# Optimization experiments

Hardware: AMD Instinct MI355X
Metric: run time of the kernel (lower is better)

Reference implementation:

```python
import jax, jax.numpy as jnp
import numpy as np

B, T = 64, 256
E = 300          # embedding_size
H = 512          # hidden_num
L = 9            # label_size
V = 30000        # vocab_size
S = 30000        # sentence_size


def setup_inputs() -> dict:
    key = jax.random.key(0)
    ks = jax.random.split(key, 14)
    D = 2 * E
    inp = {
        "text": jax.random.randint(ks[0], (B, T), 0, V, dtype=jnp.int32),
        "sentence": jax.random.randint(ks[1], (B, T), 0, S, dtype=jnp.int32),
        "labels": jax.random.randint(ks[2], (B, T), 0, L, dtype=jnp.int32),
        "word_emb": jax.random.normal(ks[3], (V, E), jnp.float32) * 0.05,
        "sent_emb": jax.random.normal(ks[4], (S, E), jnp.float32) * 0.05,
        "Wk_f": jax.random.normal(ks[5], (D, 4 * H), jnp.float32) / np.sqrt(D).astype(np.float32),
        "Wr_f": jax.random.normal(ks[6], (H, 4 * H), jnp.float32) / np.sqrt(H).astype(np.float32),
        "b_f": jnp.zeros((4 * H,), jnp.float32),
        "Wk_b": jax.random.normal(ks[7], (D, 4 * H), jnp.float32) / np.sqrt(D).astype(np.float32),
        "Wr_b": jax.random.normal(ks[8], (H, 4 * H), jnp.float32) / np.sqrt(H).astype(np.float32),
        "b_b": jnp.zeros((4 * H,), jnp.float32),
        "Wd": jax.random.normal(ks[9], (2 * H, L), jnp.float32) / np.sqrt(2 * H).astype(np.float32),
        "bd": jnp.zeros((L,), jnp.float32),
        "trans": jax.random.uniform(ks[10], (L, L), jnp.float32),
    }
    return inp


def lstm(x, Wk, Wr, b):
    # x: [B,T,D]; Keras LSTM gate order i,f,g,o; sigmoid recurrent act, tanh act.
    xz = jnp.einsum('btd,dk->btk', x, Wk) + b  # one big GEMM for all timesteps
    h0 = jnp.zeros((x.shape[0], Wr.shape[0]), x.dtype)

    def step(carry, z_t):
        h, c = carry
        z = z_t + h @ Wr
        i, f, g, o = jnp.split(z, 4, axis=-1)
        c = jax.nn.sigmoid(f) * c + jax.nn.sigmoid(i) * jnp.tanh(g)
        h = jax.nn.sigmoid(o) * jnp.tanh(c)
        return (h, c), h

    _, hs = jax.lax.scan(step, (h0, h0), jnp.swapaxes(xz, 0, 1))
    return jnp.swapaxes(hs, 0, 1)  # [B,T,H]


def crf_log_likelihood(logits, labels, mask, trans):
    maskf = mask.astype(logits.dtype)
    # unary score of the gold path
    unary = jnp.take_along_axis(logits, labels[..., None], axis=-1)[..., 0]  # [B,T]
    unary = jnp.sum(unary * maskf, axis=-1)
    # binary (transition) score
    binary = trans[labels[:, :-1], labels[:, 1:]]  # [B,T-1]
    binary = jnp.sum(binary * maskf[:, 1:], axis=-1)
    # forward algorithm (log partition), masked steps carry alpha
    logits_tm = jnp.swapaxes(logits, 0, 1)  # [T,B,L]
    mask_tm = jnp.swapaxes(mask, 0, 1)

    def step(alpha, inputs):
        logit_t, m_t = inputs
        new = jax.nn.logsumexp(alpha[:, :, None] + trans[None], axis=1) + logit_t
        return jnp.where(m_t[:, None], new, alpha), None

    alpha, _ = jax.lax.scan(step, logits_tm[0], (logits_tm[1:], mask_tm[1:]))
    log_norm = jax.nn.logsumexp(alpha, axis=-1)
    return unary + binary - log_norm


def crf_decode(logits, trans, mask):
    b, t, l = logits.shape
    logits_tm = jnp.swapaxes(logits, 0, 1)
    mask_tm = jnp.swapaxes(mask, 0, 1)
    ident = jnp.broadcast_to(jnp.arange(l)[None], (b, l))

    def step(alpha, inputs):
        logit_t, m_t = inputs
        score = alpha[:, :, None] + trans[None]      # [B,L,L]
        bp = jnp.argmax(score, axis=1)               # [B,L]
        new = jnp.max(score, axis=1) + logit_t
        alpha = jnp.where(m_t[:, None], new, alpha)
        bp = jnp.where(m_t[:, None], bp, ident)      # identity through padding
        return alpha, bp

    alpha, bps = jax.lax.scan(step, logits_tm[0], (logits_tm[1:], mask_tm[1:]))
    last = jnp.argmax(alpha, axis=-1)  # [B]

    def back(tag, bp):
        prev = jnp.take_along_axis(bp, tag[:, None], axis=1)[:, 0]
        return prev, prev

    _, tags = jax.lax.scan(back, last, bps, reverse=True)  # [T-1,B], original time order
    tags = jnp.concatenate([tags, last[None]], axis=0)     # [T,B]
    return jnp.swapaxes(tags, 0, 1).astype(jnp.int32)


def reference(text, sentence, labels, word_emb, sent_emb, Wk_f, Wr_f, b_f,
              Wk_b, Wr_b, b_b, Wd, bd, trans):
    x = jnp.concatenate([word_emb[text], sent_emb[sentence]], axis=-1)  # [B,T,2E]
    hf = lstm(x, Wk_f, Wr_f, b_f)
    hb = lstm(x[:, ::-1], Wk_b, Wr_b, b_b)[:, ::-1]
    h = jnp.concatenate([hf, hb], axis=-1)  # [B,T,2H]
    logits = h @ Wd + bd                    # [B,T,L]
    text_lens = jnp.sum((text != 0).astype(jnp.int32), axis=-1)
    mask = jnp.arange(T)[None, :] < text_lens[:, None]
    log_likelihood = crf_log_likelihood(logits, labels, mask, trans)
    pred_tags = crf_decode(logits, trans, mask)
    return logits, text_lens, log_likelihood, pred_tags
```

## Files before the change

kernel.cpp:

```cpp
#include <hip/hip_runtime.h>
#include <hip/hip_bf16.h>
#include <math.h>

#define BB 64
#define TT 256
#define EE 300
#define DD 600
#define KP 608
#define HH 512
#define G4 2048
#define LL 9
#define NT (BB*TT)

typedef __attribute__((ext_vector_type(8))) short short8;
typedef __attribute__((ext_vector_type(4))) float floatx4;

#define XZF_OFF  ((size_t)0)
#define XZ_BYTES ((size_t)NT * G4 * 2)
#define XZB_OFF  (XZF_OFF + XZ_BYTES)
#define HSR_OFF  (XZB_OFF + XZ_BYTES)
#define HS_BYTES ((size_t)NT * HH * 2)
#define HSF_OFF  (HSR_OFF)
#define HSB_OFF  (HSR_OFF + HS_BYTES)
#define XG_OFF   (HSR_OFF)
#define WKT_OFF  (HSR_OFF + 19922944)
#define WRT_OFF  (HSR_OFF + (size_t)2 * HS_BYTES)
#define BK_OFF   (WRT_OFF + 4194304)
#define FAST_OFF (BK_OFF + 524288)
#define EX_BYTES ((size_t)2 * 2 * BB * HH * 4)
#define FLAGS_OFF (FAST_OFF + 524288)
#define WDT_OFF  XZF_OFF

#define OUT_LOGITS 0
#define OUT_LENS   (BB*TT*LL)
#define OUT_LL     (OUT_LENS + BB)
#define OUT_TAGS   (OUT_LL + BB)

__global__ __launch_bounds__(256) void prep_xg(
    const int* __restrict__ text, const int* __restrict__ sent,
    const float* __restrict__ wemb, const float* __restrict__ semb,
    __hip_bfloat16* __restrict__ xg)
{
    int n = blockIdx.x;
    int ti = text[n], si = sent[n];
    __hip_bfloat16* o = xg + (size_t)n * KP;
    for (int k = threadIdx.x; k < KP; k += 256) {
        float v = 0.f;
        if (k < EE)      v = wemb[(size_t)ti * EE + k];
        else if (k < DD) v = semb[(size_t)si * EE + (k - EE)];
        o[k] = __float2bfloat16(v);
    }
}

__global__ __launch_bounds__(256) void transpose_w(
    const float* __restrict__ Wf, const float* __restrict__ Wb,
    __hip_bfloat16* __restrict__ outT, int Din, int Dpad)
{
    int dir = blockIdx.z;
    const float* W = dir ? Wb : Wf;
    __hip_bfloat16* o = outT + (size_t)dir * G4 * Dpad;
    int n0 = blockIdx.x * 64, d0 = blockIdx.y * 64;
    __shared__ float tile[64][65];
    int c = threadIdx.x & 63, r4 = threadIdx.x >> 6;
    #pragma unroll
    for (int rr = 0; rr < 64; rr += 4) {
        int d = d0 + rr + r4;
        tile[rr + r4][c] = (d < Din) ? W[(size_t)d * G4 + n0 + c] : 0.f;
    }
    __syncthreads();
    #pragma unroll
    for (int rr = 0; rr < 64; rr += 4) {
        int n = n0 + rr + r4;
        int d = d0 + c;
        if (d < Dpad) o[(size_t)n * Dpad + d] = __float2bfloat16(tile[c][rr + r4]);
    }
}

__global__ __launch_bounds__(256) void prep_wdT(
    const float* __restrict__ Wd, __hip_bfloat16* __restrict__ WdT)
{
    for (int i = threadIdx.x + blockIdx.x * 256; i < 16 * 1024; i += gridDim.x * 256) {
        int nn = i >> 10, k = i & 1023;
        WdT[i] = __float2bfloat16(nn < LL ? Wd[(size_t)k * LL + nn] : 0.f);
    }
}

__global__ __launch_bounds__(256) void embed_gemm(
    const __hip_bfloat16* __restrict__ xg,
    const __hip_bfloat16* __restrict__ WkT,
    const float* __restrict__ b_f, const float* __restrict__ b_b,
    __hip_bfloat16* __restrict__ xz_f, __hip_bfloat16* __restrict__ xz_b)
{
    int dir = blockIdx.z;
    const __hip_bfloat16* wt = WkT + (size_t)dir * G4 * KP;
    const float* bias = dir ? b_b : b_f;
    __hip_bfloat16* xz = dir ? xz_b : xz_f;

    int n0 = blockIdx.x * 128;
    int c0 = blockIdx.y * 64;
    int wave = threadIdx.x >> 6, lane = threadIdx.x & 63;
    int m0 = (wave & 1) * 64;
    int nn0 = (wave >> 1) * 32;
    int lm = lane & 15, lk8 = (lane >> 4) * 8;

    const short8 *ap[4], *bp2[2];
    #pragma unroll
    for (int i = 0; i < 4; ++i)
        ap[i] = (const short8*)(xg + (size_t)(n0 + m0 + i*16 + lm) * KP + lk8);
    #pragma unroll
    for (int i = 0; i < 2; ++i)
        bp2[i] = (const short8*)(wt + (size_t)(c0 + nn0 + i*16 + lm) * KP + lk8);

    floatx4 acc[4][2] = {};
    for (int kc = 0; kc < KP/32; ++kc) {
        short8 a0 = ap[0][kc*4], a1 = ap[1][kc*4], a2 = ap[2][kc*4], a3 = ap[3][kc*4];
        short8 b0 = bp2[0][kc*4], b1 = bp2[1][kc*4];
        acc[0][0] = __builtin_amdgcn_mfma_f32_16x16x32_bf16(a0, b0, acc[0][0], 0,0,0);
        acc[0][1] = __builtin_amdgcn_mfma_f32_16x16x32_bf16(a0, b1, acc[0][1], 0,0,0);
        acc[1][0] = __builtin_amdgcn_mfma_f32_16x16x32_bf16(a1, b0, acc[1][0], 0,0,0);
        acc[1][1] = __builtin_amdgcn_mfma_f32_16x16x32_bf16(a1, b1, acc[1][1], 0,0,0);
        acc[2][0] = __builtin_amdgcn_mfma_f32_16x16x32_bf16(a2, b0, acc[2][0], 0,0,0);
        acc[2][1] = __builtin_amdgcn_mfma_f32_16x16x32_bf16(a2, b1, acc[2][1], 0,0,0);
        acc[3][0] = __builtin_amdgcn_mfma_f32_16x16x32_bf16(a3, b0, acc[3][0], 0,0,0);
        acc[3][1] = __builtin_amdgcn_mfma_f32_16x16x32_bf16(a3, b1, acc[3][1], 0,0,0);
    }

    int lr = (lane >> 4) * 4;
    #pragma unroll
    for (int ni = 0; ni < 2; ++ni) {
        int col = c0 + nn0 + ni*16 + lm;
        float bs = bias[col];
        #pragma unroll
        for (int mi = 0; mi < 4; ++mi) {
            #pragma unroll
            for (int r = 0; r < 4; ++r) {
                int row = n0 + m0 + mi*16 + lr + r;
                xz[(size_t)row * G4 + col] = __float2bfloat16(acc[mi][ni][r] + bs);
            }
        }
    }
}

__device__ __forceinline__ void load16_sc0(const unsigned long long* base,
                                           int tid, unsigned long long* v)
{
    #pragma unroll
    for (int q = 0; q < 16; ++q) {
        const unsigned long long* ap = base + tid + 256 * q;
        asm volatile("global_load_dwordx2 %0, %1, off sc0"
                     : "=v"(v[q]) : "v"(ap));
    }
    asm volatile("s_waitcnt vmcnt(0)" ::: "memory");
}

__device__ __forceinline__ void store_sc0(unsigned long long* p,
                                          unsigned long long val)
{
    asm volatile("global_store_dwordx2 %0, %1, off sc0"
                 :: "v"(p), "v"(val) : "memory");
}

__device__ __forceinline__ unsigned load_u32_sc0(const unsigned* p)
{
    unsigned r;
    asm volatile("global_load_dword %0, %1, off sc0\n\ts_waitcnt vmcnt(0)"
                 : "=v"(r) : "v"(p) : "memory");
    return r;
}

__device__ __forceinline__ void store_u32_sc0(unsigned* p, unsigned v)
{
    asm volatile("global_store_dword %0, %1, off sc0" :: "v"(p), "v"(v) : "memory");
}

__device__ __forceinline__ void block_barrier_raw()
{
    asm volatile("" ::: "memory");
    __builtin_amdgcn_sched_barrier(0);
    __builtin_amdgcn_s_barrier();
    __builtin_amdgcn_sched_barrier(0);
    asm volatile("" ::: "memory");
}

__global__ __launch_bounds__(256, 1) void lstm_coop(
    const __hip_bfloat16* __restrict__ xz_f, const __hip_bfloat16* __restrict__ xz_b,
    const __hip_bfloat16* __restrict__ WrT,
    unsigned* __restrict__ bk,
    unsigned* __restrict__ fast,
    unsigned* __restrict__ flags,
    __hip_bfloat16* __restrict__ hs_f, __hip_bfloat16* __restrict__ hs_b)
{
    int blk = blockIdx.x;
    int g = blk & 7;
    int member = blk >> 3;
    int dir = g >> 2;
    int r0 = (g & 3) * 16;
    int h0 = member * 16;
    int tid = threadIdx.x;
    int gate = tid >> 6, lane = tid & 63;
    int lm = lane & 15, lk8 = (lane >> 4) * 8;

    const __hip_bfloat16* xz = dir ? xz_b : xz_f;
    __hip_bfloat16* hs = dir ? hs_b : hs_f;
    const __hip_bfloat16* wrt = WrT + (size_t)dir * G4 * HH;
    unsigned* bkd = bk + (size_t)dir * 2 * BB * HH;
    unsigned* fsd = fast + (size_t)dir * 2 * BB * HH;
    const unsigned* gfl = flags + (g << 5);
    unsigned* myflag = flags + (g << 5) + member;

    short8 bfrag[16];
    {
        const short8* wp = (const short8*)(wrt + (size_t)(gate*HH + h0 + lm) * HH + lk8);
        #pragma unroll
        for (int kc = 0; kc < 16; ++kc) bfrag[kc] = wp[kc*4];
    }

    __shared__ unsigned short htile[16][520];
    __shared__ float zbuf[4][16][17];

    int er = tid >> 3, ec = (tid & 7) * 2;
    float c0st = 0.f, c1st = 0.f;
    int zr = (lane >> 4) * 4;

    unsigned short xz_cur[4], xz_nxt[4];
    {
        int tok0 = dir ? (TT - 1) : 0;
        #pragma unroll
        for (int r = 0; r < 4; ++r) {
            int n = (r0 + zr + r) * TT + tok0;
            xz_cur[r] = *(const unsigned short*)(xz + (size_t)n * G4 + gate*HH + h0 + lm);
        }
    }

    bool fastok = true;
    int fallcnt = 0;

    for (int t = 0; t < TT; ++t) {
        int tok = dir ? (TT - 1 - t) : t;
        size_t soff = (size_t)(t & 1) * BB * HH + (size_t)r0 * HH;
        const unsigned long long pat =
            ((unsigned long long)(unsigned)t << 48) |
            ((unsigned long long)(unsigned)t << 16);

        unsigned long long v[16];
        bool ok = false;
        if (fastok) {
            const unsigned long long* fsrc = (const unsigned long long*)(fsd + soff);
            load16_sc0(fsrc, tid, v);
            unsigned long long bad = 0;
            #pragma unroll
            for (int q = 0; q < 16; ++q)
                bad |= (v[q] ^ pat) & 0xFFFF0000FFFF0000ULL;
            if (__all(bad == 0)) {
                ok = true;
            } else {
                unsigned need = (unsigned)t;
                bool flagok = false;
                for (int spin = 0; spin < 96; ++spin) {
                    unsigned f = load_u32_sc0(gfl + (lane & 31));
                    if (__all(f >= need)) { flagok = true; break; }
                    __builtin_amdgcn_s_sleep(2);
                }
                if (flagok) {
                    load16_sc0(fsrc, tid, v);
                    bad = 0;
                    #pragma unroll
                    for (int q = 0; q < 16; ++q)
                        bad |= (v[q] ^ pat) & 0xFFFF0000FFFF0000ULL;
                    if (__all(bad == 0)) ok = true;
                }
                if (!ok) { if (++fallcnt >= 3) fastok = false; }
            }
        }
        if (!ok) {
            const unsigned long long* bsrc = (const unsigned long long*)(bkd + soff);
            for (;;) {
                #pragma unroll
                for (int q = 0; q < 16; ++q)
                    v[q] = __hip_atomic_load(bsrc + tid + 256*q,
                            __ATOMIC_RELAXED, __HIP_MEMORY_SCOPE_AGENT);
                unsigned long long bad = 0;
                #pragma unroll
                for (int q = 0; q < 16; ++q)
                    bad |= (v[q] ^ pat) & 0xFFFF0000FFFF0000ULL;
                if (bad == 0) break;
                __builtin_amdgcn_s_sleep(2);
            }
        }

        #pragma unroll
        for (int q = 0; q < 16; ++q) {
            unsigned lo = (unsigned)(v[q] & 0xffffu);
            unsigned hi = (unsigned)((v[q] >> 32) & 0xffffu);
            *(unsigned*)&htile[q][tid * 2] = lo | (hi << 16);
        }
        __syncthreads();

        if (t + 1 < TT) {
            int tokn = dir ? (TT - 2 - t) : (t + 1);
            #pragma unroll
            for (int r = 0; r < 4; ++r) {
                int n = (r0 + zr + r) * TT + tokn;
                xz_nxt[r] = *(const unsigned short*)(xz + (size_t)n * G4 + gate*HH + h0 + lm);
            }
        }

        floatx4 acc = {};
        #pragma unroll
        for (int kc = 0; kc < 16; ++kc) {
            short8 a = *(const short8*)&htile[lm][kc * 32 + lk8];
            acc = __builtin_amdgcn_mfma_f32_16x16x32_bf16(a, bfrag[kc], acc, 0,0,0);
        }

        #pragma unroll
        for (int r = 0; r < 4; ++r) {
            float xv = __bfloat162float(__builtin_bit_cast(__hip_bfloat16, xz_cur[r]));
            zbuf[gate][zr + r][lm] = acc[r] + xv;
        }

        asm volatile("s_waitcnt lgkmcnt(0)" ::: "memory");
        block_barrier_raw();

        if (tid < 128) {
            float zi0 = zbuf[0][er][ec],   zi1 = zbuf[0][er][ec+1];
            float zf0 = zbuf[1][er][ec],   zf1 = zbuf[1][er][ec+1];
            float zg0 = zbuf[2][er][ec],   zg1 = zbuf[2][er][ec+1];
            float zo0 = zbuf[3][er][ec],   zo1 = zbuf[3][er][ec+1];
            float si0 = 1.f/(1.f+__expf(-zi0)), si1 = 1.f/(1.f+__expf(-zi1));
            float sf0 = 1.f/(1.f+__expf(-zf0)), sf1 = 1.f/(1.f+__expf(-zf1));
            float so0 = 1.f/(1.f+__expf(-zo0)), so1 = 1.f/(1.f+__expf(-zo1));
            c0st = sf0 * c0st + si0 * tanhf(zg0);
            c1st = sf1 * c1st + si1 * tanhf(zg1);
            float h0v = so0 * tanhf(c0st);
            float h1v = so1 * tanhf(c1st);
            unsigned u0 = (unsigned)__builtin_bit_cast(unsigned short, __float2bfloat16(h0v));
            unsigned u1 = (unsigned)__builtin_bit_cast(unsigned short, __float2bfloat16(h1v));
            unsigned tg = (unsigned)(t + 1) << 16;
            unsigned long long pay =
                ((unsigned long long)(tg | u1) << 32) | (unsigned long long)(tg | u0);
            size_t eoff = (size_t)((t+1) & 1) * BB * HH + (size_t)(r0 + er) * HH + h0 + ec;
            store_sc0((unsigned long long*)(fsd + eoff), pay);
            asm volatile("s_waitcnt vmcnt(0)" ::: "memory");
            __hip_atomic_store((unsigned long long*)(bkd + eoff), pay,
                               __ATOMIC_RELAXED, __HIP_MEMORY_SCOPE_AGENT);
            *(unsigned*)(hs + ((size_t)(r0 + er) * TT + tok) * HH + h0 + ec) =
                u0 | (u1 << 16);
        }
        block_barrier_raw();
        if (tid == 0)
            store_u32_sc0(myflag, (unsigned)(t + 1));

        #pragma unroll
        for (int r = 0; r < 4; ++r) xz_cur[r] = xz_nxt[r];
    }
}

__global__ __launch_bounds__(256) void logits_kernel(
    const __hip_bfloat16* __restrict__ hs_f, const __hip_bfloat16* __restrict__ hs_b,
    const __hip_bfloat16* __restrict__ WdT, const float* __restrict__ bd,
    float* __restrict__ out)
{
    int n0 = blockIdx.x * 64;
    int wave = threadIdx.x >> 6, lane = threadIdx.x & 63;
    int lm = lane & 15, lk8 = (lane >> 4) * 8;
    int nw = n0 + wave * 16;
    const short8* af = (const short8*)(hs_f + (size_t)(nw + lm) * HH + lk8);
    const short8* ab = (const short8*)(hs_b + (size_t)(nw + lm) * HH + lk8);
    const short8* bw = (const short8*)(WdT + (size_t)lm * 1024 + lk8);
    floatx4 acc = {};
    #pragma unroll
    for (int kc = 0; kc < 16; ++kc) {
        acc = __builtin_amdgcn_mfma_f32_16x16x32_bf16(af[kc*4], bw[kc*4], acc, 0,0,0);
        acc = __builtin_amdgcn_mfma_f32_16x16x32_bf16(ab[kc*4], bw[(kc+16)*4], acc, 0,0,0);
    }
    if (lm < LL) {
        float bv = bd[lm];
        #pragma unroll
        for (int r = 0; r < 4; ++r) {
            int n = nw + (lane >> 4) * 4 + r;
            out[(size_t)n * LL + lm] = acc[r] + bv;
        }
    }
}

__global__ __launch_bounds__(256) void crf_kernel(
    const float* __restrict__ logits, const int* __restrict__ text,
    const int* __restrict__ labels, const float* __restrict__ trans,
    float* __restrict__ out_lens, float* __restrict__ out_ll,
    float* __restrict__ out_tags)
{
    int b = blockIdx.x, tid = threadIdx.x;
    const float* lg = logits + (size_t)b * TT * LL;
    const int* lab = labels + b * TT;

    __shared__ float lgs[TT * LL];
    __shared__ float trs[81];
    __shared__ unsigned char bps[255 * LL + 1];
    __shared__ float partial[256];
    __shared__ int ired[256];
    __shared__ float tagf[TT];

    for (int i = tid; i < TT * LL; i += 256) lgs[i] = lg[i];
    if (tid < 81) trs[tid] = trans[tid];
    ired[tid] = (text[b * TT + tid] != 0) ? 1 : 0;
    __syncthreads();
    for (int s = 128; s > 0; s >>= 1) {
        if (tid < s) ired[tid] += ired[tid + s];
        __syncthreads();
    }
    int len = ired[0];
    if (tid == 0) out_lens[b] = (float)len;

    float up = 0.f;
    for (int t = tid; t < TT; t += 256) {
        float m = (t < len) ? 1.f : 0.f;
        up += m * lgs[t * LL + lab[t]];
        if (t >= 1) up += m * trs[lab[t - 1] * LL + lab[t]];
    }
    partial[tid] = up;
    __syncthreads();
    for (int s = 128; s > 0; s >>= 1) {
        if (tid < s) partial[tid] += partial[tid + s];
        __syncthreads();
    }

    if (tid < 64) {
        int lane = tid;
        int j = (lane < LL) ? lane : 0;
        float trj[LL];
        #pragma unroll
        for (int i = 0; i < LL; ++i) trj[i] = trs[i * LL + j];
        float alpha = lgs[j];
        float vit = alpha;
        for (int t = 1; t < TT; ++t) {
            bool m = t < len;
            float lgv = lgs[t * LL + j];
            float ta[LL];
            float mx = -1e30f, bv = -1e30f; int bi = 0;
            #pragma unroll
            for (int i = 0; i < LL; ++i) {
                float av = __shfl(alpha, i);
                float vv = __shfl(vit, i);
                ta[i] = av + trj[i];
                mx = fmaxf(mx, ta[i]);
                float sv = vv + trj[i];
                if (sv > bv) { bv = sv; bi = i; }
            }
            float s = 0.f;
            #pragma unroll
            for (int i = 0; i < LL; ++i) s += __expf(ta[i] - mx);
            float newa = mx + __logf(s) + lgv;
            float newv = bv + lgv;
            if (m) { alpha = newa; vit = newv; }
            if (lane < LL) bps[(t - 1) * LL + lane] = (unsigned char)(m ? bi : lane);
        }
        float aX[LL], vX[LL];
        #pragma unroll
        for (int i = 0; i < LL; ++i) { aX[i] = __shfl(alpha, i); vX[i] = __shfl(vit, i); }
        if (lane == 0) {
            float mx = -1e30f;
            #pragma unroll
            for (int i = 0; i < LL; ++i) mx = fmaxf(mx, aX[i]);
            float s = 0.f;
            #pragma unroll
            for (int i = 0; i < LL; ++i) s += __expf(aX[i] - mx);
            out_ll[b] = partial[0] - (mx + __logf(s));

            float bvv = vX[0]; int last = 0;
            #pragma unroll
            for (int i = 1; i < LL; ++i) if (vX[i] > bvv) { bvv = vX[i]; last = i; }
            tagf[TT - 1] = (float)last;
            int tg = last;
            for (int s2 = TT - 2; s2 >= 0; --s2) {
                tg = bps[s2 * LL + tg];
                tagf[s2] = (float)tg;
            }
        }
    }
    __syncthreads();
    out_tags[b * TT + tid] = tagf[tid];
}

extern "C" void kernel_launch(void* const* d_in, const int* in_sizes, int n_in,
                              void* d_out, int out_size, void* d_ws, size_t ws_size,
                              hipStream_t stream)
{
    const int*   text  = (const int*)d_in[0];
    const int*   sent  = (const int*)d_in[1];
    const int*   labels= (const int*)d_in[2];
    const float* wemb  = (const float*)d_in[3];
    const float* semb  = (const float*)d_in[4];
    const float* Wk_f  = (const float*)d_in[5];
    const float* Wr_f  = (const float*)d_in[6];
    const float* b_f   = (const float*)d_in[7];
    const float* Wk_b  = (const float*)d_in[8];
    const float* Wr_b  = (const float*)d_in[9];
    const float* b_b   = (const float*)d_in[10];
    const float* Wd    = (const float*)d_in[11];
    const float* bd    = (const float*)d_in[12];
    const float* trans = (const float*)d_in[13];
    float* out = (float*)d_out;

    char* ws = (char*)d_ws;
    __hip_bfloat16* xz_f = (__hip_bfloat16*)(ws + XZF_OFF);
    __hip_bfloat16* xz_b = (__hip_bfloat16*)(ws + XZB_OFF);
    __hip_bfloat16* hs_f = (__hip_bfloat16*)(ws + HSF_OFF);
    __hip_bfloat16* hs_b = (__hip_bfloat16*)(ws + HSB_OFF);
    __hip_bfloat16* xg   = (__hip_bfloat16*)(ws + XG_OFF);
    __hip_bfloat16* WkT  = (__hip_bfloat16*)(ws + WKT_OFF);
    __hip_bfloat16* WrT  = (__hip_bfloat16*)(ws + WRT_OFF);
    unsigned*       bk   = (unsigned*)(ws + BK_OFF);
    unsigned*       fast = (unsigned*)(ws + FAST_OFF);
    unsigned*       flg  = (unsigned*)(ws + FLAGS_OFF);
    __hip_bfloat16* WdT  = (__hip_bfloat16*)(ws + WDT_OFF);

    prep_xg <<<NT,  256, 0, stream>>>(text, sent, wemb, semb, xg);
    transpose_w<<<dim3(G4/64, (KP+63)/64, 2), 256, 0, stream>>>(Wk_f, Wk_b, WkT, DD, KP);
    transpose_w<<<dim3(G4/64, HH/64, 2),      256, 0, stream>>>(Wr_f, Wr_b, WrT, HH, HH);
    hipMemsetAsync(ws + BK_OFF, 0, 2 * EX_BYTES + 1024, stream);

    embed_gemm<<<dim3(NT/128, G4/64, 2), 256, 0, stream>>>(
        xg, WkT, b_f, b_b, xz_f, xz_b);

    {
        void* args[] = { (void*)&xz_f, (void*)&xz_b, (void*)&WrT,
                         (void*)&bk, (void*)&fast, (void*)&flg,
                         (void*)&hs_f, (void*)&hs_b };
        hipLaunchCooperativeKernel((const void*)lstm_coop, dim3(256), dim3(256),
                                   args, 0, stream);
    }

    prep_wdT<<<16, 256, 0, stream>>>(Wd, WdT);
    logits_kernel<<<NT/64, 256, 0, stream>>>(hs_f, hs_b, WdT, bd, out + OUT_LOGITS);
    crf_kernel<<<BB, 256, 0, stream>>>(out + OUT_LOGITS, text, labels, trans,
                                       out + OUT_LENS, out + OUT_LL, out + OUT_TAGS);
}
```

Before: 1.533 ms.

## Repartition LSTM recurrence into fewer, wider blocks of 512 threads

The cooperative LSTM kernel moves from 256 blocks of 256 threads, each owning 16 hidden units, to 64 blocks of 512 threads, each owning 64 hidden units. Every wave now issues two MFMA chains over 32 hidden columns, and all threads take part in the gate nonlinearities. With 8 members per group instead of 32, fewer blocks have to publish and poll per timestep, which is meant to cut cross-block synchronisation latency. In exchange each block does more serial work per step and holds more registers for weights. The fast-path fallback counter also now resets after a successful step.

```diff
diff --git a/kernel.cpp b/kernel.cpp
--- a/kernel.cpp
+++ b/kernel.cpp
@@ -141,12 +141,12 @@
     }
 }
 
-__device__ __forceinline__ void load16_sc0(const unsigned long long* base,
-                                           int tid, unsigned long long* v)
-{
-    #pragma unroll
-    for (int q = 0; q < 16; ++q) {
-        const unsigned long long* ap = base + tid + 256 * q;
+__device__ __forceinline__ void load8_sc0(const unsigned long long* base,
+                                          int tid, unsigned long long* v)
+{
+    #pragma unroll
+    for (int q = 0; q < 8; ++q) {
+        const unsigned long long* ap = base + tid + 512 * q;
         asm volatile("global_load_dwordx2 %0, %1, off sc0"
                      : "=v"(v[q]) : "v"(ap));
     }
@@ -182,7 +182,7 @@
     asm volatile("" ::: "memory");
 }
 
-__global__ __launch_bounds__(256, 1) void lstm_coop(
+__global__ __launch_bounds__(512, 2) void lstm_coop(
     const __hip_bfloat16* __restrict__ xz_f, const __hip_bfloat16* __restrict__ xz_b,
     const __hip_bfloat16* __restrict__ WrT,
     unsigned* __restrict__ bk,
@@ -195,10 +195,13 @@
     int member = blk >> 3;
     int dir = g >> 2;
     int r0 = (g & 3) * 16;
-    int h0 = member * 16;
     int tid = threadIdx.x;
-    int gate = tid >> 6, lane = tid & 63;
+    int wave = tid >> 6, lane = tid & 63;
+    int gate = wave >> 1;
+    int chunk = wave & 1;
     int lm = lane & 15, lk8 = (lane >> 4) * 8;
+    int zr = (lane >> 4) * 4;
+    int hbase = member * 64 + chunk * 32;
 
     const __hip_bfloat16* xz = dir ? xz_b : xz_f;
     __hip_bfloat16* hs = dir ? hs_b : hs_f;
@@ -208,28 +211,34 @@
     const unsigned* gfl = flags + (g << 5);
     unsigned* myflag = flags + (g << 5) + member;
 
-    short8 bfrag[16];
+    short8 bfragA[16], bfragB[16];
     {
-        const short8* wp = (const short8*)(wrt + (size_t)(gate*HH + h0 + lm) * HH + lk8);
-        #pragma unroll
-        for (int kc = 0; kc < 16; ++kc) bfrag[kc] = wp[kc*4];
+        const short8* wpA = (const short8*)(wrt +
+            (size_t)(gate*HH + hbase + lm) * HH + lk8);
+        const short8* wpB = (const short8*)(wrt +
+            (size_t)(gate*HH + hbase + 16 + lm) * HH + lk8);
+        #pragma unroll
+        for (int kc = 0; kc < 16; ++kc) { bfragA[kc] = wpA[kc*4]; bfragB[kc] = wpB[kc*4]; }
     }
 
     __shared__ unsigned short htile[16][520];
-    __shared__ float zbuf[4][16][17];
-
-    int er = tid >> 3, ec = (tid & 7) * 2;
+    __shared__ float zbuf[4][16][66];
+
+    int er = tid >> 5;
+    int ec = (tid & 31) * 2;
     float c0st = 0.f, c1st = 0.f;
-    int zr = (lane >> 4) * 4;
-
-    unsigned short xz_cur[4], xz_nxt[4];
+
+    unsigned short xz_cur[8], xz_nxt[8];
     {
         int tok0 = dir ? (TT - 1) : 0;
         #pragma unroll
-        for (int r = 0; r < 4; ++r) {
-            int n = (r0 + zr + r) * TT + tok0;
-            xz_cur[r] = *(const unsigned short*)(xz + (size_t)n * G4 + gate*HH + h0 + lm);
-        }
+        for (int ni = 0; ni < 2; ++ni)
+            #pragma unroll
+            for (int r = 0; r < 4; ++r) {
+                int n = (r0 + zr + r) * TT + tok0;
+                xz_cur[ni*4 + r] = *(const unsigned short*)(
+                    xz + (size_t)n * G4 + gate*HH + hbase + ni*16 + lm);
+            }
     }
 
     bool fastok = true;
@@ -242,14 +251,14 @@
             ((unsigned long long)(unsigned)t << 48) |
             ((unsigned long long)(unsigned)t << 16);
 
-        unsigned long long v[16];
+        unsigned long long v[8];
         bool ok = false;
         if (fastok) {
             const unsigned long long* fsrc = (const unsigned long long*)(fsd + soff);
-            load16_sc0(fsrc, tid, v);
+            load8_sc0(fsrc, tid, v);
             unsigned long long bad = 0;
             #pragma unroll
-            for (int q = 0; q < 16; ++q)
+            for (int q = 0; q < 8; ++q)
                 bad |= (v[q] ^ pat) & 0xFFFF0000FFFF0000ULL;
             if (__all(bad == 0)) {
                 ok = true;
@@ -257,71 +266,81 @@
                 unsigned need = (unsigned)t;
                 bool flagok = false;
                 for (int spin = 0; spin < 96; ++spin) {
-                    unsigned f = load_u32_sc0(gfl + (lane & 31));
+                    unsigned f = load_u32_sc0(gfl + (lane & 7));
                     if (__all(f >= need)) { flagok = true; break; }
                     __builtin_amdgcn_s_sleep(2);
                 }
                 if (flagok) {
-                    load16_sc0(fsrc, tid, v);
+                    load8_sc0(fsrc, tid, v);
                     bad = 0;
                     #pragma unroll
-                    for (int q = 0; q < 16; ++q)
+                    for (int q = 0; q < 8; ++q)
                         bad |= (v[q] ^ pat) & 0xFFFF0000FFFF0000ULL;
                     if (__all(bad == 0)) ok = true;
                 }
-                if (!ok) { if (++fallcnt >= 3) fastok = false; }
-            }
+            }
+            if (ok) fallcnt = 0;
+            else if (++fallcnt >= 3) fastok = false;
         }
         if (!ok) {
             const unsigned long long* bsrc = (const unsigned long long*)(bkd + soff);
             for (;;) {
                 #pragma unroll
-                for (int q = 0; q < 16; ++q)
-                    v[q] = __hip_atomic_load(bsrc + tid + 256*q,
+                for (int q = 0; q < 8; ++q)
+                    v[q] = __hip_atomic_load(bsrc + tid + 512*q,
                             __ATOMIC_RELAXED, __HIP_MEMORY_SCOPE_AGENT);
                 unsigned long long bad = 0;
                 #pragma unroll
-                for (int q = 0; q < 16; ++q)
+                for (int q = 0; q < 8; ++q)
                     bad |= (v[q] ^ pat) & 0xFFFF0000FFFF0000ULL;
                 if (bad == 0) break;
                 __builtin_amdgcn_s_sleep(2);
             }
         }
 
-        #pragma unroll
-        for (int q = 0; q < 16; ++q) {
-            unsigned lo = (unsigned)(v[q] & 0xffffu);
-            unsigned hi = (unsigned)((v[q] >> 32) & 0xffffu);
-            *(unsigned*)&htile[q][tid * 2] = lo | (hi << 16);
+        {
+            int srow = tid >> 8, scol = (tid & 255) * 2;
+            #pragma unroll
+            for (int q = 0; q < 8; ++q) {
+                unsigned lo = (unsigned)(v[q] & 0xffffu);
+                unsigned hi = (unsigned)((v[q] >> 32) & 0xffffu);
+                *(unsigned*)&htile[2*q + srow][scol] = lo | (hi << 16);
+            }
         }
         __syncthreads();
 
         if (t + 1 < TT) {
             int tokn = dir ? (TT - 2 - t) : (t + 1);
             #pragma unroll
-            for (int r = 0; r < 4; ++r) {
-                int n = (r0 + zr + r) * TT + tokn;
-                xz_nxt[r] = *(const unsigned short*)(xz + (size_t)n * G4 + gate*HH + h0 + lm);
-            }
-        }
-
-        floatx4 acc = {};
+            for (int ni = 0; ni < 2; ++ni)
+                #pragma unroll
+                for (int r = 0; r < 4; ++r) {
+                    int n = (r0 + zr + r) * TT + tokn;
+                    xz_nxt[ni*4 + r] = *(const unsigned short*)(
+                        xz + (size_t)n * G4 + gate*HH + hbase + ni*16 + lm);
+                }
+        }
+
+        floatx4 accA = {}, accB = {};
         #pragma unroll
         for (int kc = 0; kc < 16; ++kc) {
             short8 a = *(const short8*)&htile[lm][kc * 32 + lk8];
-            acc = __builtin_amdgcn_mfma_f32_16x16x32_bf16(a, bfrag[kc], acc, 0,0,0);
+            accA = __builtin_amdgcn_mfma_f32_16x16x32_bf16(a, bfragA[kc], accA, 0,0,0);
+            accB = __builtin_amdgcn_mfma_f32_16x16x32_bf16(a, bfragB[kc], accB, 0,0,0);
         }
 
         #pragma unroll
         for (int r = 0; r < 4; ++r) {
-            float xv = __bfloat162float(__builtin_bit_cast(__hip_bfloat16, xz_cur[r]));
-            zbuf[gate][zr + r][lm] = acc[r] + xv;
+            float xvA = __bfloat162float(__builtin_bit_cast(__hip_bfloat16, xz_cur[r]));
+            float xvB = __bfloat162float(__builtin_bit_cast(__hip_bfloat16, xz_cur[4 + r]));
+            zbuf[gate][zr + r][chunk*32 + lm]      = accA[r] + xvA;
+            zbuf[gate][zr + r][chunk*32 + 16 + lm] = accB[r] + xvB;
         }
 
         asm volatile("s_waitcnt lgkmcnt(0)" ::: "memory");
         block_barrier_raw();
 
-        if (tid < 128) {
+        {
             float zi0 = zbuf[0][er][ec],   zi1 = zbuf[0][er][ec+1];
             float zf0 = zbuf[1][er][ec],   zf1 = zbuf[1][er][ec+1];
             float zg0 = zbuf[2][er][ec],   zg1 = zbuf[2][er][ec+1];
@@ -338,12 +357,13 @@
             unsigned tg = (unsigned)(t + 1) << 16;
             unsigned long long pay =
                 ((unsigned long long)(tg | u1) << 32) | (unsigned long long)(tg | u0);
-            size_t eoff = (size_t)((t+1) & 1) * BB * HH + (size_t)(r0 + er) * HH + h0 + ec;
+            size_t eoff = (size_t)((t+1) & 1) * BB * HH
+                        + (size_t)(r0 + er) * HH + member*64 + ec;
             store_sc0((unsigned long long*)(fsd + eoff), pay);
             asm volatile("s_waitcnt vmcnt(0)" ::: "memory");
             __hip_atomic_store((unsigned long long*)(bkd + eoff), pay,
                                __ATOMIC_RELAXED, __HIP_MEMORY_SCOPE_AGENT);
-            *(unsigned*)(hs + ((size_t)(r0 + er) * TT + tok) * HH + h0 + ec) =
+            *(unsigned*)(hs + ((size_t)(r0 + er) * TT + tok) * HH + member*64 + ec) =
                 u0 | (u1 << 16);
         }
         block_barrier_raw();
@@ -351,7 +371,7 @@
             store_u32_sc0(myflag, (unsigned)(t + 1));
 
         #pragma unroll
-        for (int r = 0; r < 4; ++r) xz_cur[r] = xz_nxt[r];
+        for (int i = 0; i < 8; ++i) xz_cur[i] = xz_nxt[i];
     }
 }
 
@@ -526,7 +546,7 @@
         void* args[] = { (void*)&xz_f, (void*)&xz_b, (void*)&WrT,
                          (void*)&bk, (void*)&fast, (void*)&flg,
                          (void*)&hs_f, (void*)&hs_b };
-        hipLaunchCooperativeKernel((const void*)lstm_coop, dim3(256), dim3(256),
+        hipLaunchCooperativeKernel((const void*)lstm_coop, dim3(64), dim3(512),
                                    args, 0, stream);
     }
 
```

Result: slower. 2.737 ms (+78.6%).

## Use flag-gated packed bf16 exchange with dwordx4 loads in LSTM recurrence

Applied to the files above, without the earlier changes.

The fast path of the persistent LSTM recurrence now waits on per-group step flags first, then reads a packed bf16 h buffer with no embedded step tags using four 16-byte loads per thread. The old path read sixteen 8-byte tagged words and validated them. The gate nonlinearity is also spread over all 256 threads, one column each, with lane shuffles to pair outputs, where before 128 threads handled two columns each. The aim is to halve exchange traffic and shorten the per-step critical path. Correctness now depends on flag ordering, since data stores must be visible before the flag store, and the polling is tighter.

```diff
diff --git a/kernel.cpp b/kernel.cpp
--- a/kernel.cpp
+++ b/kernel.cpp
@@ -14,6 +14,7 @@
 
 typedef __attribute__((ext_vector_type(8))) short short8;
 typedef __attribute__((ext_vector_type(4))) float floatx4;
+typedef __attribute__((ext_vector_type(4))) unsigned uintx4;
 
 #define XZF_OFF  ((size_t)0)
 #define XZ_BYTES ((size_t)NT * G4 * 2)
@@ -141,23 +142,15 @@
     }
 }
 
-__device__ __forceinline__ void load16_sc0(const unsigned long long* base,
-                                           int tid, unsigned long long* v)
-{
-    #pragma unroll
-    for (int q = 0; q < 16; ++q) {
-        const unsigned long long* ap = base + tid + 256 * q;
-        asm volatile("global_load_dwordx2 %0, %1, off sc0"
+__device__ __forceinline__ void load4x16_sc0(const char* base, int tid, uintx4* v)
+{
+    #pragma unroll
+    for (int q = 0; q < 4; ++q) {
+        const char* ap = base + (size_t)(tid + 256 * q) * 16;
+        asm volatile("global_load_dwordx4 %0, %1, off sc0"
                      : "=v"(v[q]) : "v"(ap));
     }
     asm volatile("s_waitcnt vmcnt(0)" ::: "memory");
-}
-
-__device__ __forceinline__ void store_sc0(unsigned long long* p,
-                                          unsigned long long val)
-{
-    asm volatile("global_store_dwordx2 %0, %1, off sc0"
-                 :: "v"(p), "v"(val) : "memory");
 }
 
 __device__ __forceinline__ unsigned load_u32_sc0(const unsigned* p)
@@ -204,7 +197,7 @@
     __hip_bfloat16* hs = dir ? hs_b : hs_f;
     const __hip_bfloat16* wrt = WrT + (size_t)dir * G4 * HH;
     unsigned* bkd = bk + (size_t)dir * 2 * BB * HH;
-    unsigned* fsd = fast + (size_t)dir * 2 * BB * HH;
+    char* fsd = (char*)fast + (size_t)dir * 2 * BB * HH * 2;
     const unsigned* gfl = flags + (g << 5);
     unsigned* myflag = flags + (g << 5) + member;
 
@@ -218,8 +211,9 @@
     __shared__ unsigned short htile[16][520];
     __shared__ float zbuf[4][16][17];
 
-    int er = tid >> 3, ec = (tid & 7) * 2;
-    float c0st = 0.f, c1st = 0.f;
+    int er = tid >> 4;
+    int ecol = tid & 15;
+    float cst = 0.f;
     int zr = (lane >> 4) * 4;
 
     unsigned short xz_cur[4], xz_nxt[4];
@@ -235,45 +229,41 @@
     bool fastok = true;
     int fallcnt = 0;
 
+    int frow = tid >> 6;
+    int fcol = (tid & 63) * 8;
+
     for (int t = 0; t < TT; ++t) {
         int tok = dir ? (TT - 1 - t) : t;
-        size_t soff = (size_t)(t & 1) * BB * HH + (size_t)r0 * HH;
         const unsigned long long pat =
             ((unsigned long long)(unsigned)t << 48) |
             ((unsigned long long)(unsigned)t << 16);
 
-        unsigned long long v[16];
         bool ok = false;
         if (fastok) {
-            const unsigned long long* fsrc = (const unsigned long long*)(fsd + soff);
-            load16_sc0(fsrc, tid, v);
-            unsigned long long bad = 0;
-            #pragma unroll
-            for (int q = 0; q < 16; ++q)
-                bad |= (v[q] ^ pat) & 0xFFFF0000FFFF0000ULL;
-            if (__all(bad == 0)) {
+            unsigned need = (unsigned)t;
+            bool flagok = false;
+            for (int spin = 0; spin < 256; ++spin) {
+                unsigned f = load_u32_sc0(gfl + (lane & 31));
+                if (__all(f >= need)) { flagok = true; break; }
+                __builtin_amdgcn_s_sleep(1);
+            }
+            if (flagok) {
+                const char* fsrc = fsd + (size_t)(t & 1) * 65536 + (size_t)r0 * 1024;
+                uintx4 v4[4];
+                load4x16_sc0(fsrc, tid, v4);
+                #pragma unroll
+                for (int q = 0; q < 4; ++q)
+                    *(uintx4*)&htile[frow + 4*q][fcol] = v4[q];
                 ok = true;
-            } else {
-                unsigned need = (unsigned)t;
-                bool flagok = false;
-                for (int spin = 0; spin < 96; ++spin) {
-                    unsigned f = load_u32_sc0(gfl + (lane & 31));
-                    if (__all(f >= need)) { flagok = true; break; }
-                    __builtin_amdgcn_s_sleep(2);
-                }
-                if (flagok) {
-                    load16_sc0(fsrc, tid, v);
-                    bad = 0;
-                    #pragma unroll
-                    for (int q = 0; q < 16; ++q)
-                        bad |= (v[q] ^ pat) & 0xFFFF0000FFFF0000ULL;
-                    if (__all(bad == 0)) ok = true;
-                }
-                if (!ok) { if (++fallcnt >= 3) fastok = false; }
+                fallcnt = 0;
+            } else if (++fallcnt >= 3) {
+                fastok = false;
             }
         }
         if (!ok) {
+            size_t soff = (size_t)(t & 1) * BB * HH + (size_t)r0 * HH;
             const unsigned long long* bsrc = (const unsigned long long*)(bkd + soff);
+            unsigned long long v[16];
             for (;;) {
                 #pragma unroll
                 for (int q = 0; q < 16; ++q)
@@ -286,13 +276,12 @@
                 if (bad == 0) break;
                 __builtin_amdgcn_s_sleep(2);
             }
-        }
-
-        #pragma unroll
-        for (int q = 0; q < 16; ++q) {
-            unsigned lo = (unsigned)(v[q] & 0xffffu);
-            unsigned hi = (unsigned)((v[q] >> 32) & 0xffffu);
-            *(unsigned*)&htile[q][tid * 2] = lo | (hi << 16);
+            #pragma unroll
+            for (int q = 0; q < 16; ++q) {
+                unsigned lo = (unsigned)(v[q] & 0xffffu);
+                unsigned hi = (unsigned)((v[q] >> 32) & 0xffffu);
+                *(unsigned*)&htile[q][tid * 2] = lo | (hi << 16);
+            }
         }
         __syncthreads();
 
@@ -321,30 +310,35 @@
         asm volatile("s_waitcnt lgkmcnt(0)" ::: "memory");
         block_barrier_raw();
 
-        if (tid < 128) {
-            float zi0 = zbuf[0][er][ec],   zi1 = zbuf[0][er][ec+1];
-            float zf0 = zbuf[1][er][ec],   zf1 = zbuf[1][er][ec+1];
-            float zg0 = zbuf[2][er][ec],   zg1 = zbuf[2][er][ec+1];
-            float zo0 = zbuf[3][er][ec],   zo1 = zbuf[3][er][ec+1];
-            float si0 = 1.f/(1.f+__expf(-zi0)), si1 = 1.f/(1.f+__expf(-zi1));
-            float sf0 = 1.f/(1.f+__expf(-zf0)), sf1 = 1.f/(1.f+__expf(-zf1));
-            float so0 = 1.f/(1.f+__expf(-zo0)), so1 = 1.f/(1.f+__expf(-zo1));
-            c0st = sf0 * c0st + si0 * tanhf(zg0);
-            c1st = sf1 * c1st + si1 * tanhf(zg1);
-            float h0v = so0 * tanhf(c0st);
-            float h1v = so1 * tanhf(c1st);
-            unsigned u0 = (unsigned)__builtin_bit_cast(unsigned short, __float2bfloat16(h0v));
-            unsigned u1 = (unsigned)__builtin_bit_cast(unsigned short, __float2bfloat16(h1v));
-            unsigned tg = (unsigned)(t + 1) << 16;
-            unsigned long long pay =
-                ((unsigned long long)(tg | u1) << 32) | (unsigned long long)(tg | u0);
-            size_t eoff = (size_t)((t+1) & 1) * BB * HH + (size_t)(r0 + er) * HH + h0 + ec;
-            store_sc0((unsigned long long*)(fsd + eoff), pay);
-            asm volatile("s_waitcnt vmcnt(0)" ::: "memory");
-            __hip_atomic_store((unsigned long long*)(bkd + eoff), pay,
-                               __ATOMIC_RELAXED, __HIP_MEMORY_SCOPE_AGENT);
-            *(unsigned*)(hs + ((size_t)(r0 + er) * TT + tok) * HH + h0 + ec) =
-                u0 | (u1 << 16);
+        {
+            float zi = zbuf[0][er][ecol];
+            float zf = zbuf[1][er][ecol];
+            float zg = zbuf[2][er][ecol];
+            float zo = zbuf[3][er][ecol];
+            float si = 1.f/(1.f+__expf(-zi));
+            float sf = 1.f/(1.f+__expf(-zf));
+            float so = 1.f/(1.f+__expf(-zo));
+            cst = sf * cst + si * tanhf(zg);
+            float hv = so * tanhf(cst);
+            unsigned u = (unsigned)__builtin_bit_cast(unsigned short, __float2bfloat16(hv));
+            unsigned un = __shfl_down(u, 1);
+            if ((tid & 1) == 0) {
+                unsigned dpay = u | (un << 16);
+                unsigned tg = (unsigned)(t + 1) << 16;
+                unsigned long long bpay =
+                    ((unsigned long long)(tg | un) << 32) | (unsigned long long)(tg | u);
+                int slot = (t + 1) & 1;
+                int col = h0 + ecol;
+                store_u32_sc0((unsigned*)(fsd + (size_t)slot * 65536
+                                          + (size_t)(r0 + er) * 1024 + col * 2), dpay);
+                asm volatile("s_waitcnt vmcnt(0)" ::: "memory");
+                size_t eoff = (size_t)slot * BB * HH + (size_t)(r0 + er) * HH + col;
+                __hip_atomic_store((unsigned long long*)(bkd + eoff), bpay,
+                                   __ATOMIC_RELAXED, __HIP_MEMORY_SCOPE_AGENT);
+                *(unsigned*)(hs + ((size_t)(r0 + er) * TT + tok) * HH + col) = dpay;
+            } else {
+                asm volatile("s_waitcnt vmcnt(0)" ::: "memory");
+            }
         }
         block_barrier_raw();
         if (tid == 0)
```

New measurement: 5.733 ms. +274.0%, slower.
